# Performance work log

Hardware: AMD Instinct MI355X
Metric: run time of the kernel (lower is better)

Reference implementation:

```python
import jax, jax.numpy as jnp
import numpy as np

N, M, P = 8192, 8192, 16


def setup_inputs() -> dict:
    key = jax.random.key(0)
    k1, k2, k3, k4, k5 = jax.random.split(key, 5)
    x1 = jax.random.normal(k1, (N, P), dtype=jnp.float32)
    x2 = jax.random.normal(k2, (M, P), dtype=jnp.float32)
    # flax initializers.uniform() draws in [0, 0.01); use small scalars
    log_sigma_b = jax.random.uniform(k3, (), dtype=jnp.float32) * 0.01
    log_sigma_v = jax.random.uniform(k4, (), dtype=jnp.float32) * 0.01
    offset = jax.random.uniform(k5, (), dtype=jnp.float32) * 0.01
    return {"x1": x1, "x2": x2, "log_sigma_b": log_sigma_b,
            "log_sigma_v": log_sigma_v, "offset": offset}


def reference(x1, x2, log_sigma_b, log_sigma_v, offset):
    sigma_b = jnp.exp(log_sigma_b)
    sigma_v = jnp.exp(log_sigma_v)
    # sum_p (x1-offset)(x2-offset) as a dot product (n,p)@(p,m) -> (n,m)
    d = jnp.einsum("np,mp->nm", x1 - offset, x2 - offset)
    K = sigma_v ** 2 * d + sigma_b ** 2
    return K
```

## Files before the change

### kernel.cpp

```cpp
#include <hip/hip_runtime.h>
#include <cmath>


typedef float f32x4 __attribute__((ext_vector_type(4)));

#define ROWS_PER_BLOCK 32
#define BLOCK_COLS 1024

__global__ __launch_bounds__(256, 4) void linear_kernel(
    const float* __restrict__ x1, const float* __restrict__ x2,
    const float* __restrict__ p_lsb, const float* __restrict__ p_lsv,
    const float* __restrict__ p_off, float* __restrict__ out,
    int n, int m)
{
    const int lane = threadIdx.x & 63;
    const int wid  = __builtin_amdgcn_readfirstlane(threadIdx.x >> 6);
    const int c0   = blockIdx.x * BLOCK_COLS + wid * 256 + (lane << 2);
    const int n0   = blockIdx.y * ROWS_PER_BLOCK;

    const float off = p_off[0];
    const float sv  = expf(p_lsv[0]);
    const float sb  = expf(p_lsb[0]);
    const float sv2 = sv * sv;
    const float sb2 = sb * sb;

    float C[4][16];
    float bias[4];
    #pragma unroll
    for (int c = 0; c < 4; ++c) {
        const f32x4* g = (const f32x4*)(x2 + (size_t)(c0 + c) * 16);
        float s = 0.0f;
        #pragma unroll
        for (int q = 0; q < 4; ++q) {
            f32x4 v = g[q];
            #pragma unroll
            for (int j = 0; j < 4; ++j) {
                const float t = sv2 * (v[j] - off);
                C[c][q * 4 + j] = t;
                s += t;
            }
        }
        bias[c] = sb2 - off * s;
    }

    float* orow = out + (size_t)n0 * m + c0;
    const f32x4* arow = (const f32x4*)(x1 + (size_t)n0 * 16);
    #pragma unroll 2
    for (int r = 0; r < ROWS_PER_BLOCK; ++r) {
        const f32x4 a0 = arow[0];
        const f32x4 a1 = arow[1];
        const f32x4 a2 = arow[2];
        const f32x4 a3 = arow[3];
        float a[16];
        #pragma unroll
        for (int j = 0; j < 4; ++j) {
            a[j]      = a0[j];
            a[4 + j]  = a1[j];
            a[8 + j]  = a2[j];
            a[12 + j] = a3[j];
        }
        f32x4 acc;
        acc[0] = bias[0]; acc[1] = bias[1]; acc[2] = bias[2]; acc[3] = bias[3];
        #pragma unroll
        for (int p = 0; p < 16; ++p) {
            acc[0] = fmaf(a[p], C[0][p], acc[0]);
            acc[1] = fmaf(a[p], C[1][p], acc[1]);
            acc[2] = fmaf(a[p], C[2][p], acc[2]);
            acc[3] = fmaf(a[p], C[3][p], acc[3]);
        }
        *(f32x4*)orow = acc;
        orow += m;
        arow += 4;
    }
}

extern "C" void kernel_launch(void* const* d_in, const int* in_sizes, int n_in,
                              void* d_out, int out_size, void* d_ws, size_t ws_size,
                              hipStream_t stream) {
    const float* x1  = (const float*)d_in[0];
    const float* x2  = (const float*)d_in[1];
    const float* lsb = (const float*)d_in[2];
    const float* lsv = (const float*)d_in[3];
    const float* off = (const float*)d_in[4];
    float* out = (float*)d_out;

    const int n = in_sizes[0] / 16;
    const int m = in_sizes[1] / 16;

    dim3 grid(m / BLOCK_COLS, n / ROWS_PER_BLOCK);
    linear_kernel<<<grid, 256, 0, stream>>>(x1, x2, lsb, lsv, off, out, n, m);
}
```

Baseline: 291.3 us.

## Switch to 64x64 LDS-tiled outer-product kernel with 4x4 register blocking

```diff
diff --git a/kernel.cpp b/kernel.cpp
--- a/kernel.cpp
+++ b/kernel.cpp
@@ -4,73 +4,69 @@
 
 typedef float f32x4 __attribute__((ext_vector_type(4)));
 
-#define ROWS_PER_BLOCK 32
-#define BLOCK_COLS 1024
+#define TILE 64
+#define LDST 68
 
-__global__ __launch_bounds__(256, 4) void linear_kernel(
+__global__ __launch_bounds__(256, 8) void linear_kernel(
     const float* __restrict__ x1, const float* __restrict__ x2,
     const float* __restrict__ p_lsb, const float* __restrict__ p_lsv,
-    const float* __restrict__ p_off, float* __restrict__ out,
-    int n, int m)
+    const float* __restrict__ p_off, float* __restrict__ out, int m)
 {
-    const int lane = threadIdx.x & 63;
-    const int wid  = __builtin_amdgcn_readfirstlane(threadIdx.x >> 6);
-    const int c0   = blockIdx.x * BLOCK_COLS + wid * 256 + (lane << 2);
-    const int n0   = blockIdx.y * ROWS_PER_BLOCK;
+    __shared__ float s1[16 * LDST];
+    __shared__ float s2[16 * LDST];
+
+    const int tid = threadIdx.x;
+    const int tx  = tid & 15;
+    const int ty  = tid >> 4;
+    const int n0  = blockIdx.y * TILE;
+    const int m0  = blockIdx.x * TILE;
 
     const float off = p_off[0];
     const float sv  = expf(p_lsv[0]);
     const float sb  = expf(p_lsb[0]);
-    const float sv2 = sv * sv;
     const float sb2 = sb * sb;
 
-    float C[4][16];
-    float bias[4];
-    #pragma unroll
-    for (int c = 0; c < 4; ++c) {
-        const f32x4* g = (const f32x4*)(x2 + (size_t)(c0 + c) * 16);
-        float s = 0.0f;
+    {
+        const int row = tid >> 2;
+        const int q   = tid & 3;
+        const f32x4 v = ((const f32x4*)(x1 + (size_t)(n0 + row) * 16))[q];
+        const f32x4 w = ((const f32x4*)(x2 + (size_t)(m0 + row) * 16))[q];
         #pragma unroll
-        for (int q = 0; q < 4; ++q) {
-            f32x4 v = g[q];
-            #pragma unroll
-            for (int j = 0; j < 4; ++j) {
-                const float t = sv2 * (v[j] - off);
-                C[c][q * 4 + j] = t;
-                s += t;
-            }
+        for (int j = 0; j < 4; ++j) {
+            s1[(q * 4 + j) * LDST + row] = sv * (v[j] - off);
+            s2[(q * 4 + j) * LDST + row] = sv * (w[j] - off);
         }
-        bias[c] = sb2 - off * s;
     }
 
-    float* orow = out + (size_t)n0 * m + c0;
-    const f32x4* arow = (const f32x4*)(x1 + (size_t)n0 * 16);
-    #pragma unroll 2
-    for (int r = 0; r < ROWS_PER_BLOCK; ++r) {
-        const f32x4 a0 = arow[0];
-        const f32x4 a1 = arow[1];
-        const f32x4 a2 = arow[2];
-        const f32x4 a3 = arow[3];
-        float a[16];
+    float acc[4][4];
+    #pragma unroll
+    for (int r = 0; r < 4; ++r)
         #pragma unroll
-        for (int j = 0; j < 4; ++j) {
-            a[j]      = a0[j];
-            a[4 + j]  = a1[j];
-            a[8 + j]  = a2[j];
-            a[12 + j] = a3[j];
-        }
-        f32x4 acc;
-        acc[0] = bias[0]; acc[1] = bias[1]; acc[2] = bias[2]; acc[3] = bias[3];
+        for (int c = 0; c < 4; ++c) acc[r][c] = 0.0f;
+
+    __syncthreads();
+
+    #pragma unroll
+    for (int p = 0; p < 16; ++p) {
+        const f32x4 a4 = *(const f32x4*)&s1[p * LDST + ty * 4];
+        const f32x4 b4 = *(const f32x4*)&s2[p * LDST + tx * 4];
         #pragma unroll
-        for (int p = 0; p < 16; ++p) {
-            acc[0] = fmaf(a[p], C[0][p], acc[0]);
-            acc[1] = fmaf(a[p], C[1][p], acc[1]);
-            acc[2] = fmaf(a[p], C[2][p], acc[2]);
-            acc[3] = fmaf(a[p], C[3][p], acc[3]);
-        }
-        *(f32x4*)orow = acc;
+        for (int r = 0; r < 4; ++r)
+            #pragma unroll
+            for (int c = 0; c < 4; ++c)
+                acc[r][c] = fmaf(a4[r], b4[c], acc[r][c]);
+    }
+
+    float* orow = out + (size_t)(n0 + ty * 4) * m + m0 + tx * 4;
+    #pragma unroll
+    for (int r = 0; r < 4; ++r) {
+        f32x4 o;
+        o[0] = acc[r][0] + sb2;
+        o[1] = acc[r][1] + sb2;
+        o[2] = acc[r][2] + sb2;
+        o[3] = acc[r][3] + sb2;
+        *(f32x4*)orow = o;
         orow += m;
-        arow += 4;
     }
 }
 
@@ -87,6 +83,6 @@
     const int n = in_sizes[0] / 16;
     const int m = in_sizes[1] / 16;
 
-    dim3 grid(m / BLOCK_COLS, n / ROWS_PER_BLOCK);
-    linear_kernel<<<grid, 256, 0, stream>>>(x1, x2, lsb, lsv, off, out, n, m);
+    dim3 grid(m / TILE, n / TILE);
+    linear_kernel<<<grid, 256, 0, stream>>>(x1, x2, lsb, lsv, off, out, m);
 }
```

Result: slower. 335.5 us (+15.2%).
